# Kernel tuning notes

Measured on AMD Instinct MI355X. Metric: run time of the kernel, lower is better.

The kernel has to match this reference:

```python
import jax, jax.numpy as jnp
import numpy as np

V = 100000   # nodes (atoms)
E = 400000   # directed edges (bonds x2)
N = 74       # node_feat_size
NE = 12      # edge_feat_size
G = 200      # graph_feat_size
L = 2        # num_layers - 1 GNN layers
OUT = 1      # output_size
NG = 4000    # molecules in the batch


def _lin_init(k, fan_in, fan_out):
    s = 1.0 / np.sqrt(fan_in)
    return jax.random.uniform(k, (fan_in, fan_out), jnp.float32, -s, s)


def setup_inputs() -> dict:
    key = jax.random.key(0)
    ks = list(jax.random.split(key, 40))
    p = {}
    # node feats uniform in (0.05, 0.95) so mask = 1/(sum(h[:,-4:])*(1-h[:,0])) - 1 is finite
    p["node_feats"] = jax.random.uniform(ks[0], (V, N), jnp.float32, 0.05, 0.95)
    p["edge_feats"] = jax.random.normal(ks[1], (E, NE), jnp.float32)
    # GetContext params
    p["pn_W"] = _lin_init(ks[2], N, G);            p["pn_b"] = jnp.zeros((G,), jnp.float32)
    p["pe1_W"] = _lin_init(ks[3], N + NE, G);      p["pe1_b"] = jnp.zeros((G,), jnp.float32)
    p["pe2_W"] = _lin_init(ks[4], 2 * G, 1);       p["pe2_b"] = jnp.zeros((1,), jnp.float32)
    p["et_W"] = _lin_init(ks[5], G, G);            p["et_b"] = jnp.zeros((G,), jnp.float32)
    p["gru0_Wih"] = _lin_init(ks[6], G, 3 * G);    p["gru0_Whh"] = _lin_init(ks[7], G, 3 * G)
    p["gru0_bih"] = jnp.zeros((3 * G,), jnp.float32)
    p["gru0_bhh"] = jnp.zeros((3 * G,), jnp.float32)
    # stacked GNNLayer params
    p["gnn_pe_W"] = jnp.stack([_lin_init(ks[8 + l], 2 * G, 1) for l in range(L)])
    p["gnn_pe_b"] = jnp.zeros((L, 1), jnp.float32)
    p["gnn_pn_W"] = jnp.stack([_lin_init(ks[10 + l], G, G) for l in range(L)])
    p["gnn_pn_b"] = jnp.zeros((L, G), jnp.float32)
    p["gnn_gru_Wih"] = jnp.stack([_lin_init(ks[12 + l], G, 3 * G) for l in range(L)])
    p["gnn_gru_Whh"] = jnp.stack([_lin_init(ks[14 + l], G, 3 * G) for l in range(L)])
    p["gnn_gru_bih"] = jnp.zeros((L, 3 * G), jnp.float32)
    p["gnn_gru_bhh"] = jnp.zeros((L, 3 * G), jnp.float32)
    p["pred_W"] = _lin_init(ks[16], G, OUT);       p["pred_b"] = jnp.zeros((OUT,), jnp.float32)
    # graph structure
    p["src"] = jax.random.randint(ks[17], (E,), 0, V)
    p["dst"] = jax.random.randint(ks[18], (E,), 0, V)
    p["graph_ids"] = jnp.arange(V, dtype=jnp.int32) // (V // NG)  # sorted, balanced, non-empty
    p["n_graphs"] = NG
    return p


def _edge_softmax(logits, dst, num_nodes):
    # softmax over incoming edges of each destination node (DGL edge_softmax)
    m = jax.ops.segment_max(logits, dst, num_segments=num_nodes)
    e = jnp.exp(logits - m[dst])
    s = jax.ops.segment_sum(e, dst, num_segments=num_nodes)
    return e / s[dst]


def _gru_cell(x, h, Wih, Whh, bih, bhh):
    gi = x @ Wih + bih
    gh = h @ Whh + bhh
    ir, iz, inn = jnp.split(gi, 3, axis=-1)
    hr, hz, hn = jnp.split(gh, 3, axis=-1)
    r = jax.nn.sigmoid(ir + hr)
    z = jax.nn.sigmoid(iz + hz)
    n = jnp.tanh(inn + r * hn)
    return (1.0 - z) * n + z * h


def _forward(node_feats, edge_feats, pn_W, pn_b, pe1_W, pe1_b, pe2_W, pe2_b,
             et_W, et_b, gru0_Wih, gru0_Whh, gru0_bih, gru0_bhh,
             gnn_pe_W, gnn_pe_b, gnn_pn_W, gnn_pn_b,
             gnn_gru_Wih, gnn_gru_Whh, gnn_gru_bih, gnn_gru_bhh,
             pred_W, pred_b, src, dst, graph_ids, n_graphs):
    Vn = node_feats.shape[0]
    lrelu = jax.nn.leaky_relu  # slope 0.01, matches torch default
    # mask from original node features g.ndata['h']
    mask = jnp.sum(node_feats[:, -4:], axis=1) * (1.0 - node_feats[:, 0])
    mask = 1.0 / mask - 1.0
    # --- GetContext ---
    hv_new = lrelu(node_feats @ pn_W + pn_b)                               # (V, G)
    he1 = lrelu(jnp.concatenate([node_feats[src], edge_feats], 1) @ pe1_W + pe1_b)  # (E, G)
    he2 = jnp.concatenate([hv_new[dst], he1], 1)                           # (E, 2G)
    logits = lrelu(he2 @ pe2_W + pe2_b)                                    # (E, 1)
    a = _edge_softmax(logits, dst, Vn)
    e = a * (he1 @ et_W + et_b)                                            # (E, G)
    c = jax.ops.segment_sum(e, dst, num_segments=Vn)                       # (V, G)
    nf = jax.nn.relu(_gru_cell(jax.nn.elu(c), hv_new,
                               gru0_Wih, gru0_Whh, gru0_bih, gru0_bhh))
    # --- GNN layers ---
    for l in range(gnn_pe_W.shape[0]):
        he = jnp.concatenate([nf[dst], nf[src]], 1)                        # (E, 2G)
        lg = lrelu(he @ gnn_pe_W[l] + gnn_pe_b[l])                         # (E, 1)
        a = _edge_softmax(lg, dst, Vn)
        hvp = nf @ gnn_pn_W[l] + gnn_pn_b[l]                               # (V, G)
        c = jax.ops.segment_sum(hvp[src] * a, dst, num_segments=Vn)        # (V, G)
        nf = jax.nn.relu(_gru_cell(jax.nn.elu(c), nf,
                                   gnn_gru_Wih[l], gnn_gru_Whh[l],
                                   gnn_gru_bih[l], gnn_gru_bhh[l]))
    # --- readout ---
    atom_pka = nf @ pred_W + pred_b                                        # (V, 1)
    atom_pka = -(atom_pka + mask[:, None])
    h_pow = jnp.power(10.0, atom_pka)
    g_feats = -jnp.log10(jax.ops.segment_sum(h_pow, graph_ids, num_segments=n_graphs))
    atom_pka_out = -atom_pka
    return g_feats, atom_pka_out


def reference(node_feats, edge_feats, pn_W, pn_b, pe1_W, pe1_b, pe2_W, pe2_b,
              et_W, et_b, gru0_Wih, gru0_Whh, gru0_bih, gru0_bhh,
              gnn_pe_W, gnn_pe_b, gnn_pn_W, gnn_pn_b,
              gnn_gru_Wih, gnn_gru_Whh, gnn_gru_bih, gnn_gru_bhh,
              pred_W, pred_b, src, dst, graph_ids, n_graphs):
    return _forward(node_feats, edge_feats, pn_W, pn_b, pe1_W, pe1_b, pe2_W, pe2_b,
                    et_W, et_b, gru0_Wih, gru0_Whh, gru0_bih, gru0_bhh,
                    gnn_pe_W, gnn_pe_b, gnn_pn_W, gnn_pn_b,
                    gnn_gru_Wih, gnn_gru_Whh, gnn_gru_bih, gnn_gru_bhh,
                    pred_W, pred_b, src, dst, graph_ids, n_graphs)
```

## Files before the change

### kernel.cpp

```cpp
#include <hip/hip_runtime.h>
#include <hip/hip_bf16.h>
#include <math.h>

#define V_N    100000
#define E_N    400000
#define NFEAT  74
#define NEFEAT 12
#define G_DIM  200
#define LDA    224
#define L_N    2
#define NG_N   4000
#define NROWB  391
#define NROWP  392
#define NSWZ   (NROWP / 8 * 56)
#define NSWZG  (NROWP / 8 * 112)

static inline int cdiv(int a, int b) { return (a + b - 1) / b; }

__device__ __forceinline__ float lrelu_f(float x) { return x > 0.f ? x : 0.01f * x; }
__device__ __forceinline__ float sigmoid_f(float x)
{
    return __builtin_amdgcn_rcpf(1.f + __expf(-x));
}
__device__ __forceinline__ float tanh_f(float x)
{
    return 1.f - 2.f * __builtin_amdgcn_rcpf(__expf(2.f * x) + 1.f);
}
__device__ __forceinline__ float elu_f(float x) { return x > 0.f ? x : __expf(x) - 1.f; }
__device__ __forceinline__ float bf2f(__hip_bfloat16 x) { return __bfloat162float(x); }
__device__ __forceinline__ float bfbits2f(short s) {
    return __uint_as_float(((unsigned)(unsigned short)s) << 16);
}

__device__ __forceinline__ short f2bf(float f) {
    __hip_bfloat16 b = __float2bfloat16(f);
    short s;
    __builtin_memcpy(&s, &b, 2);
    return s;
}

typedef short short8 __attribute__((ext_vector_type(8)));
typedef short short4v __attribute__((ext_vector_type(4)));
typedef float f32x4 __attribute__((ext_vector_type(4)));

#define MFMA16(a, b, c) __builtin_amdgcn_mfma_f32_16x16x32_bf16((a), (b), (c), 0, 0, 0)

#define GLOAD_LDS16(gp, lp) \
    __builtin_amdgcn_global_load_lds((const __attribute__((address_space(1))) void*)(gp), \
                                     (__attribute__((address_space(3))) void*)(lp), 16, 0, 0)

#define WAITVM(n) do { \
    asm volatile("s_waitcnt vmcnt(" #n ")" ::: "memory"); \
    __builtin_amdgcn_sched_barrier(0); \
} while (0)

__device__ __forceinline__ void swz_decode7(int lin, int& rowBlk, int& cb)
{
    int grp = lin / 56;
    int rem = lin % 56;
    cb = rem >> 3;
    rowBlk = grp * 8 + (rem & 7);
}

__device__ __forceinline__ void swz_decode14(int lin, int& rowBlk, int& cb)
{
    int grp = lin / 112;
    int rem = lin % 112;
    cb = rem >> 3;
    rowBlk = grp * 8 + (rem & 7);
}

__device__ __forceinline__ f32x4 qcalc(const f32x4* wef, f32x4 ef0, f32x4 ef1, f32x4 ef2)
{
    f32x4 q = ef0[0] * wef[0];
    q += ef0[1] * wef[1];
    q += ef0[2] * wef[2];
    q += ef0[3] * wef[3];
    q += ef1[0] * wef[4];
    q += ef1[1] * wef[5];
    q += ef1[2] * wef[6];
    q += ef1[3] * wef[7];
    q += ef2[0] * wef[8];
    q += ef2[1] * wef[9];
    q += ef2[2] * wef[10];
    q += ef2[3] * wef[11];
    return q;
}

__global__ __launch_bounds__(256)
void fill_kernel(float* __restrict__ p, float v, int n)
{
    int i = blockIdx.x * blockDim.x + threadIdx.x;
    if (i < n) p[i] = v;
}

__global__ __launch_bounds__(256)
void fill_int_kernel(int* __restrict__ p, int v, int n)
{
    int i = blockIdx.x * blockDim.x + threadIdx.x;
    if (i < n) p[i] = v;
}

__global__ __launch_bounds__(256)
void pad_zero_kernel(short* __restrict__ base, size_t VP)
{
    int idx = blockIdx.x * blockDim.x + threadIdx.x;
    if (idx >= 4 * V_N) return;
    int mat = idx / V_N, row = idx % V_N;
    short* p = base + (size_t)mat * VP + (long)row * LDA + G_DIM;
    short8 z = {};
    *(short8*)(p) = z;
    *(short8*)(p + 8) = z;
    *(short8*)(p + 16) = z;
}

__global__ __launch_bounds__(256)
void wprep_kernel(const float* __restrict__ W, short* __restrict__ Wp, int K, int Kpad)
{
    int idx = blockIdx.x * 256 + threadIdx.x;
    if (idx >= 256 * Kpad) return;
    int j = idx / Kpad, k = idx % Kpad;
    float v = (j < G_DIM && k < K) ? W[(long)k * G_DIM + j] : 0.f;
    Wp[idx] = f2bf(v);
}

__global__ __launch_bounds__(256)
void wprep_tiled_kernel(const float* __restrict__ W, short* __restrict__ Wp)
{
    int idx = blockIdx.x * 256 + threadIdx.x;
    if (idx >= 7 * 7 * 1024) return;
    int cb = idx / (7 * 1024);
    int r = idx % (7 * 1024);
    int st = r / 1024;
    int r2 = r % 1024;
    int cc = r2 / 32, kk = r2 % 32;
    int col = cb * 32 + cc, k = st * 32 + kk;
    float v = (col < G_DIM && k < G_DIM) ? W[(long)k * G_DIM + col] : 0.f;
    Wp[idx] = f2bf(v);
}

__global__ __launch_bounds__(256)
void gru_wprep_kernel(const float* __restrict__ Wih, const float* __restrict__ Whh,
                      short* __restrict__ Wp)
{
    int idx = blockIdx.x * 256 + threadIdx.x;
    if (idx >= 14 * 14 * 1536) return;
    int cb = idx / (14 * 1536);
    int r = idx % (14 * 1536);
    int st = r / 1536;
    int r2 = r % 1536;
    int g = r2 / 512;
    int r3 = r2 % 512;
    int cc = r3 / 32, kk = r3 % 32;
    int col = cb * 16 + cc;
    float v = 0.f;
    if (col < G_DIM) {
        if (st < 7) {
            int k = st * 32 + kk;
            if (k < G_DIM) v = Wih[(long)k * (3 * G_DIM) + g * G_DIM + col];
        } else {
            int k = (st - 7) * 32 + kk;
            if (k < G_DIM) v = Whh[(long)k * (3 * G_DIM) + g * G_DIM + col];
        }
    }
    Wp[idx] = f2bf(v);
}

__global__ __launch_bounds__(256)
void hist_kernel(const int* __restrict__ dst, int* __restrict__ deg)
{
    int e = blockIdx.x * blockDim.x + threadIdx.x;
    if (e >= E_N) return;
    atomicAdd(&deg[dst[e]], 1);
}

__global__ __launch_bounds__(256)
void scan1_kernel(const int* __restrict__ deg, int* __restrict__ rp, int* __restrict__ bsum)
{
    __shared__ int s[256];
    int tid = threadIdx.x;
    int v = blockIdx.x * 256 + tid;
    int x = (v < V_N) ? deg[v] : 0;
    s[tid] = x;
    __syncthreads();
    for (int off = 1; off < 256; off <<= 1) {
        int t = (tid >= off) ? s[tid - off] : 0;
        __syncthreads();
        s[tid] += t;
        __syncthreads();
    }
    if (v < V_N) rp[v] = s[tid] - x;
    if (tid == 255) bsum[blockIdx.x] = s[255];
}

__global__ void scan2_kernel(int* __restrict__ bsum, int* __restrict__ rp, int nb)
{
    if (threadIdx.x != 0 || blockIdx.x != 0) return;
    int acc = 0;
    for (int b = 0; b < nb; b++) { int t = bsum[b]; bsum[b] = acc; acc += t; }
    rp[V_N] = acc;
}

__global__ __launch_bounds__(256)
void scan3_kernel(int* __restrict__ rp, const int* __restrict__ bsum)
{
    int v = blockIdx.x * 256 + threadIdx.x;
    if (v < V_N) rp[v] += bsum[v >> 8];
}

__global__ __launch_bounds__(256)
void csr_fill_kernel(const int* __restrict__ dst, const int* __restrict__ rp,
                     int* __restrict__ cnt, int* __restrict__ perm)
{
    int e = blockIdx.x * blockDim.x + threadIdx.x;
    if (e >= E_N) return;
    int d = dst[e];
    int pos = rp[d] + atomicAdd(&cnt[d], 1);
    perm[pos] = e;
}

__global__ __launch_bounds__(256)
void gemm_f32a_dual_kernel(const float* __restrict__ Af32,
                           const short* __restrict__ Wp1, const float* __restrict__ b1,
                           const short* __restrict__ Wp2, const float* __restrict__ b2,
                           __hip_bfloat16* __restrict__ C1,
                           __hip_bfloat16* __restrict__ C2)
{
    __shared__ short As[64 * 40];
    __shared__ short Bs1[64 * 40];
    __shared__ short Bs2[64 * 40];
    const int tid = threadIdx.x;
    const int lane = tid & 63;
    const int w = tid >> 6;
    const int quad = lane >> 4;
    const int lm = lane & 15;
    const int rowBase = blockIdx.y * 64;
    const int j0 = blockIdx.x * 64;
    const int arow = tid >> 2;
    const int akc = (tid & 3) * 8;
    const int agrow = rowBase + arow;

    f32x4 acc1[4] = {}, acc2[4] = {};

    for (int k0 = 0; k0 < 96; k0 += 32) {
        short8 av = {};
        if (agrow < V_N) {
            int gk = k0 + akc;
            #pragma unroll
            for (int i = 0; i < 8; i++) {
                int kg = gk + i;
                av[i] = (kg < NFEAT) ? f2bf(Af32[(long)agrow * NFEAT + kg]) : (short)0;
            }
        }
        *(short8*)&As[arow * 40 + akc] = av;
        {
            int col = tid >> 2;
            *(short8*)&Bs1[col * 40 + akc] =
                *(const short8*)(Wp1 + (long)(j0 + col) * 96 + k0 + akc);
            *(short8*)&Bs2[col * 40 + akc] =
                *(const short8*)(Wp2 + (long)(j0 + col) * 96 + k0 + akc);
        }
        __syncthreads();
        short8 a = *(short8*)&As[(w * 16 + lm) * 40 + quad * 8];
        #pragma unroll
        for (int nt = 0; nt < 4; nt++) {
            short8 bb1 = *(short8*)&Bs1[(nt * 16 + lm) * 40 + quad * 8];
            short8 bb2 = *(short8*)&Bs2[(nt * 16 + lm) * 40 + quad * 8];
            acc1[nt] = MFMA16(a, bb1, acc1[nt]);
            acc2[nt] = MFMA16(a, bb2, acc2[nt]);
        }
        __syncthreads();
    }

    #pragma unroll
    for (int nt = 0; nt < 4; nt++) {
        int col = j0 + nt * 16 + lm;
        if (col >= G_DIM) continue;
        float bv1 = b1[col], bv2 = b2[col];
        #pragma unroll
        for (int r = 0; r < 4; r++) {
            int grow = rowBase + w * 16 + quad * 4 + r;
            if (grow >= V_N) continue;
            C1[(long)grow * LDA + col] = __float2bfloat16(lrelu_f(acc1[nt][r] + bv1));
            C2[(long)grow * LDA + col] = __float2bfloat16(acc2[nt][r] + bv2);
        }
    }
}

template<int EPI>
__global__ __launch_bounds__(256)
void gemm_bf16a_kernel(const __hip_bfloat16* __restrict__ Abf,
                       const short* __restrict__ Wp,
                       const float* __restrict__ bias,
                       __hip_bfloat16* __restrict__ Cbf)
{
    __shared__ short As[2][256 * 32];
    int rowBlk, cb;
    swz_decode7(blockIdx.x, rowBlk, cb);
    if (rowBlk >= NROWB) return;
    const int tid = threadIdx.x;
    const int lane = tid & 63;
    const int w = tid >> 6;
    const int quad = lane >> 4;
    const int lm = lane & 15;
    const int j0 = cb * 32;
    const int rowBase = rowBlk * 256;

    const short* WpB = Wp + (long)cb * (7 * 1024);
    const short* As_g = (const short*)Abf;
    const long aoff = (long)(rowBase + w * 64 + (lane >> 2)) * LDA + (lane & 3) * 8;
    const int bfrag = lm * 32 + quad * 8;

    auto stageA = [&](int st, int buf) {
        const int kl = st * 32;
        #pragma unroll
        for (int c = 0; c < 4; c++)
            GLOAD_LDS16(As_g + aoff + (long)c * 16 * LDA + kl,
                        &As[buf][(w * 64 + c * 16) * 32]);
    };
    auto loadB = [&](int st, short8 bf[2]) {
        const short* bp = WpB + st * 1024 + bfrag;
        #pragma unroll
        for (int nt = 0; nt < 2; nt++)
            bf[nt] = *(const short8*)(bp + nt * 512);
    };
    auto mfmaStep = [&](int buf, short8 bf[2], f32x4 acc[4][2]) {
        #pragma unroll
        for (int rt = 0; rt < 4; rt++) {
            short8 a = *(short8*)&As[buf][(w * 64 + rt * 16 + lm) * 32 + quad * 8];
            acc[rt][0] = MFMA16(a, bf[0], acc[rt][0]);
            acc[rt][1] = MFMA16(a, bf[1], acc[rt][1]);
        }
    };

    f32x4 acc[4][2] = {};
    short8 bA[2], bB[2];

    stageA(0, 0);
    loadB(0, bA);
    WAITVM(0);

    #pragma unroll 1
    for (int st = 0; st < 7; st += 2) {
        if (st + 1 < 7) {
            stageA(st + 1, 1);
            loadB(st + 1, bB);
            WAITVM(6);
        } else {
            WAITVM(0);
        }
        mfmaStep(0, bA, acc);
        if (st + 1 < 7) {
            if (st + 2 < 7) {
                stageA(st + 2, 0);
                loadB(st + 2, bA);
                WAITVM(6);
            } else {
                WAITVM(0);
            }
            mfmaStep(1, bB, acc);
        }
    }

    #pragma unroll
    for (int nt = 0; nt < 2; nt++) {
        int col = j0 + nt * 16 + lm;
        if (col >= G_DIM) continue;
        float bv = bias[col];
        #pragma unroll
        for (int rt = 0; rt < 4; rt++) {
            #pragma unroll
            for (int r = 0; r < 4; r++) {
                int grow = rowBase + w * 64 + rt * 16 + quad * 4 + r;
                if (grow >= V_N) continue;
                float v = acc[rt][nt][r] + bv;
                if (EPI == 3) v = elu_f(v);
                Cbf[(long)grow * LDA + col] = __float2bfloat16(v);
            }
        }
    }
}

__global__ __launch_bounds__(256, 3)
void gru_mfma_kernel(const __hip_bfloat16* __restrict__ xc,
                     const __hip_bfloat16* __restrict__ h,
                     const short* __restrict__ Wp,
                     const float* __restrict__ bih, const float* __restrict__ bhh,
                     __hip_bfloat16* __restrict__ out)
{
    __shared__ short As[2][256 * 32];
    int rowBlk, cb;
    swz_decode14(blockIdx.x, rowBlk, cb);
    if (rowBlk >= NROWB) return;
    const int tid = threadIdx.x;
    const int lane = tid & 63;
    const int w = tid >> 6;
    const int quad = lane >> 4;
    const int lm = lane & 15;
    const int j0 = cb * 16;
    const int rowBase = rowBlk * 256;

    const short* WpB = Wp + (long)cb * (14 * 1536);
    const short* xc_s = (const short*)xc;
    const short* h_s = (const short*)h;
    const long aoff = (long)(rowBase + w * 64 + (lane >> 2)) * LDA + (lane & 3) * 8;
    const int bfrag = lm * 32 + quad * 8;

    auto stageA = [&](int st, int buf) {
        const short* Ap = (st < 7) ? xc_s : h_s;
        const int kl = (st < 7 ? st : st - 7) * 32;
        #pragma unroll
        for (int c = 0; c < 4; c++)
            GLOAD_LDS16(Ap + aoff + (long)c * 16 * LDA + kl,
                        &As[buf][(w * 64 + c * 16) * 32]);
    };
    auto loadB = [&](int st, short8 bf[3]) {
        const short* bp = WpB + st * 1536 + bfrag;
        #pragma unroll
        for (int g = 0; g < 3; g++)
            bf[g] = *(const short8*)(bp + g * 512);
    };

    f32x4 aR[4] = {}, aZ[4] = {}, aNl[4] = {}, aNh[4] = {};

    auto mfmaStep = [&](int buf, short8 bf[3], bool lowK) {
        #pragma unroll
        for (int rt = 0; rt < 4; rt++) {
            short8 a = *(short8*)&As[buf][(w * 64 + rt * 16 + lm) * 32 + quad * 8];
            aR[rt] = MFMA16(a, bf[0], aR[rt]);
            aZ[rt] = MFMA16(a, bf[1], aZ[rt]);
            if (lowK) aNl[rt] = MFMA16(a, bf[2], aNl[rt]);
            else      aNh[rt] = MFMA16(a, bf[2], aNh[rt]);
        }
    };

    short8 bA[3], bB[3];

    stageA(0, 0);
    loadB(0, bA);
    WAITVM(0);

    #pragma unroll 1
    for (int st = 0; st < 14; st += 2) {
        stageA(st + 1, 1);
        loadB(st + 1, bB);
        WAITVM(7);
        mfmaStep(0, bA, st < 7);
        if (st + 2 < 14) {
            stageA(st + 2, 0);
            loadB(st + 2, bA);
            WAITVM(7);
        } else {
            WAITVM(0);
        }
        mfmaStep(1, bB, st + 1 < 7);
    }

    int col = j0 + lm;
    if (col < G_DIM) {
        float b_r = bih[col] + bhh[col];
        float b_z = bih[G_DIM + col] + bhh[G_DIM + col];
        float b_in = bih[2 * G_DIM + col];
        float b_hn = bhh[2 * G_DIM + col];
        #pragma unroll
        for (int rt = 0; rt < 4; rt++) {
            #pragma unroll
            for (int r = 0; r < 4; r++) {
                int grow = rowBase + w * 64 + rt * 16 + quad * 4 + r;
                if (grow >= V_N) continue;
                float rr = sigmoid_f(aR[rt][r] + b_r);
                float zz = sigmoid_f(aZ[rt][r] + b_z);
                float nn = tanh_f(aNl[rt][r] + b_in + rr * (aNh[rt][r] + b_hn));
                float hval = bf2f(h[(long)grow * LDA + col]);
                float o = (1.f - zz) * nn + zz * hval;
                out[(long)grow * LDA + col] = __float2bfloat16(o > 0.f ? o : 0.f);
            }
        }
    }
}

__global__ __launch_bounds__(256)
void node_dot2_kernel(const __hip_bfloat16* __restrict__ X,
                      const float* __restrict__ wa, const float* __restrict__ wb,
                      float* __restrict__ s1, float* __restrict__ s2)
{
    int w = threadIdx.x >> 6, lane = threadIdx.x & 63;
    int v = blockIdx.x * 4 + w;
    if (v >= V_N) return;
    int vlane = (lane < 50) ? lane : 0;
    short4v pv = *(const short4v*)((const short*)X + (long)v * LDA + vlane * 4);
    f32x4 wav = *(const f32x4*)(wa + vlane * 4);
    float a = 0.f, b = 0.f;
    #pragma unroll
    for (int u = 0; u < 4; u++) a += bfbits2f(pv[u]) * wav[u];
    if (wb) {
        f32x4 wbv = *(const f32x4*)(wb + vlane * 4);
        #pragma unroll
        for (int u = 0; u < 4; u++) b += bfbits2f(pv[u]) * wbv[u];
    }
    if (lane >= 50) { a = 0.f; b = 0.f; }
    for (int off = 32; off > 0; off >>= 1) {
        a += __shfl_down(a, off, 64);
        if (wb) b += __shfl_down(b, off, 64);
    }
    if (lane == 0) {
        s1[v] = a;
        if (wb) s2[v] = b;
    }
}

__global__ __launch_bounds__(256)
void ctx_fused_kernel(const __hip_bfloat16* __restrict__ P,
                      const float* __restrict__ efeat,
                      const int* __restrict__ src,
                      const int* __restrict__ rp, const int* __restrict__ perm,
                      const float* __restrict__ s1,
                      const float* __restrict__ pe1W,
                      const float* __restrict__ pe2W, const float* __restrict__ pe2b,
                      __hip_bfloat16* __restrict__ hbar)
{
    const int tid = threadIdx.x;
    const int w = tid >> 6, lane = tid & 63;
    const int vlane = (lane < 50) ? lane : 0;
    const int v = __builtin_amdgcn_readfirstlane(blockIdx.x * 4 + w);
    if (v >= V_N) return;
    const int b = __builtin_amdgcn_readfirstlane(rp[v]);
    const int en = __builtin_amdgcn_readfirstlane(rp[v + 1]);
    if (en == b) {
        if (lane < 50) {
            short4v z = {};
            *(short4v*)((short*)hbar + (long)v * LDA + lane * 4) = z;
        }
        return;
    }
    f32x4 wef[12];
    #pragma unroll
    for (int j = 0; j < 12; j++)
        wef[j] = *(const f32x4*)(pe1W + (long)(NFEAT + j) * G_DIM + vlane * 4);
    const f32x4 w2 = *(const f32x4*)(pe2W + G_DIM + vlane * 4);
    const float s1b = s1[v] + pe2b[0];

    float m = -INFINITY, ssum = 0.f;
    f32x4 a = {};
    for (int i = b; i < en; i++) {
        const int e = __builtin_amdgcn_readfirstlane(perm[i]);
        const int sN = __builtin_amdgcn_readfirstlane(src[e]);
        const f32x4 ef0 = *(const f32x4*)(efeat + (long)e * NEFEAT);
        const f32x4 ef1 = *(const f32x4*)(efeat + (long)e * NEFEAT + 4);
        const f32x4 ef2 = *(const f32x4*)(efeat + (long)e * NEFEAT + 8);
        const short4v pv = *(const short4v*)((const short*)P + (long)sN * LDA + vlane * 4);
        const f32x4 q = qcalc(wef, ef0, ef1, ef2);
        f32x4 he;
        #pragma unroll
        for (int u = 0; u < 4; u++) he[u] = lrelu_f(bfbits2f(pv[u]) + q[u]);
        float dot = he[0] * w2[0] + he[1] * w2[1] + he[2] * w2[2] + he[3] * w2[3];
        if (lane >= 50) dot = 0.f;
        #pragma unroll
        for (int off = 32; off > 0; off >>= 1) dot += __shfl_xor(dot, off, 64);
        const float l = lrelu_f(dot + s1b);
        if (l <= m) {
            const float wgt = __expf(l - m);
            ssum += wgt;
            #pragma unroll
            for (int u = 0; u < 4; u++) a[u] += wgt * he[u];
        } else {
            const float scale = __expf(m - l);
            ssum = ssum * scale + 1.f;
            #pragma unroll
            for (int u = 0; u < 4; u++) a[u] = a[u] * scale + he[u];
            m = l;
        }
    }
    const float inv = __builtin_amdgcn_rcpf(ssum);
    if (lane < 50) {
        short4v o;
        #pragma unroll
        for (int u = 0; u < 4; u++) o[u] = f2bf(a[u] * inv);
        *(short4v*)((short*)hbar + (long)v * LDA + lane * 4) = o;
    }
}

__global__ __launch_bounds__(256)
void gnn_fused_agg_kernel(const __hip_bfloat16* __restrict__ X,
                          const int* __restrict__ src,
                          const int* __restrict__ rp, const int* __restrict__ perm,
                          const float* __restrict__ s1, const float* __restrict__ s2,
                          const float* __restrict__ bias,
                          __hip_bfloat16* __restrict__ out)
{
    const int tid = threadIdx.x;
    const int w = tid >> 6, lane = tid & 63;
    const int vlane = (lane < 50) ? lane : 0;
    const int v = __builtin_amdgcn_readfirstlane(blockIdx.x * 4 + w);
    if (v >= V_N) return;
    const int b = __builtin_amdgcn_readfirstlane(rp[v]);
    const int en = __builtin_amdgcn_readfirstlane(rp[v + 1]);
    if (en == b) {
        if (lane < 50) {
            short4v z = {};
            *(short4v*)((short*)out + (long)v * LDA + lane * 4) = z;
        }
        return;
    }
    const float s1v = s1[v] + bias[0];
    float m = -INFINITY;
    for (int i = b; i < en; i++) {
        const int e = __builtin_amdgcn_readfirstlane(perm[i]);
        const int sN = __builtin_amdgcn_readfirstlane(src[e]);
        m = fmaxf(m, lrelu_f(s1v + s2[sN]));
    }
    f32x4 a = {};
    float ssum = 0.f;
    for (int i = b; i < en; i++) {
        const int e = __builtin_amdgcn_readfirstlane(perm[i]);
        const int sN = __builtin_amdgcn_readfirstlane(src[e]);
        const float l = lrelu_f(s1v + s2[sN]);
        const float wgt = __expf(l - m);
        ssum += wgt;
        const short4v pv = *(const short4v*)((const short*)X + (long)sN * LDA + vlane * 4);
        #pragma unroll
        for (int u = 0; u < 4; u++)
            a[u] += wgt * bfbits2f(pv[u]);
    }
    const float inv = __builtin_amdgcn_rcpf(ssum);
    if (lane < 50) {
        short4v o;
        #pragma unroll
        for (int u = 0; u < 4; u++) o[u] = f2bf(elu_f(a[u] * inv));
        *(short4v*)((short*)out + (long)v * LDA + lane * 4) = o;
    }
}

__global__ __launch_bounds__(256)
void mask_kernel(const float* __restrict__ nfeat, float* __restrict__ mask)
{
    int v = blockIdx.x * blockDim.x + threadIdx.x;
    if (v >= V_N) return;
    const float* row = nfeat + (long)v * NFEAT;
    float s = row[NFEAT - 4] + row[NFEAT - 3] + row[NFEAT - 2] + row[NFEAT - 1];
    float m = s * (1.f - row[0]);
    mask[v] = 1.f / m - 1.f;
}

__global__ __launch_bounds__(256)
void readout_kernel(const __hip_bfloat16* __restrict__ nf, const float* __restrict__ predW,
                    const float* __restrict__ predb, const float* __restrict__ mask,
                    const int* __restrict__ gid, float* __restrict__ out_atom,
                    float* __restrict__ gsum)
{
    int gtid = blockIdx.x * blockDim.x + threadIdx.x;
    int v = gtid >> 6, lane = gtid & 63;
    if (v >= V_N) return;
    int vlane = (lane < 50) ? lane : 0;
    short4v pv = *(const short4v*)((const short*)nf + (long)v * LDA + vlane * 4);
    f32x4 wv = *(const f32x4*)(predW + vlane * 4);
    float acc = 0.f;
    #pragma unroll
    for (int u = 0; u < 4; u++) acc += bfbits2f(pv[u]) * wv[u];
    if (lane >= 50) acc = 0.f;
    for (int off = 32; off > 0; off >>= 1) acc += __shfl_down(acc, off, 64);
    if (lane == 0) {
        float p = acc + predb[0] + mask[v];
        out_atom[v] = p;
        atomicAdd(&gsum[gid[v]], exp10f(-p));
    }
}

__global__ __launch_bounds__(256)
void graph_out_kernel(const float* __restrict__ gsum, float* __restrict__ out_g)
{
    int g = blockIdx.x * blockDim.x + threadIdx.x;
    if (g >= NG_N) return;
    out_g[g] = -log10f(gsum[g]);
}

extern "C" void kernel_launch(void* const* d_in, const int* in_sizes, int n_in,
                              void* d_out, int out_size, void* d_ws, size_t ws_size,
                              hipStream_t stream)
{
    const float* node_feats = (const float*)d_in[0];
    const float* edge_feats = (const float*)d_in[1];
    const float* pn_W  = (const float*)d_in[2];
    const float* pn_b  = (const float*)d_in[3];
    const float* pe1_W = (const float*)d_in[4];
    const float* pe1_b = (const float*)d_in[5];
    const float* pe2_W = (const float*)d_in[6];
    const float* pe2_b = (const float*)d_in[7];
    const float* et_W  = (const float*)d_in[8];
    const float* et_b  = (const float*)d_in[9];
    const float* gru0_Wih = (const float*)d_in[10];
    const float* gru0_Whh = (const float*)d_in[11];
    const float* gru0_bih = (const float*)d_in[12];
    const float* gru0_bhh = (const float*)d_in[13];
    const float* gnn_pe_W = (const float*)d_in[14];
    const float* gnn_pe_b = (const float*)d_in[15];
    const float* gnn_pn_W = (const float*)d_in[16];
    const float* gnn_pn_b = (const float*)d_in[17];
    const float* gnn_gru_Wih = (const float*)d_in[18];
    const float* gnn_gru_Whh = (const float*)d_in[19];
    const float* gnn_gru_bih = (const float*)d_in[20];
    const float* gnn_gru_bhh = (const float*)d_in[21];
    const float* pred_W = (const float*)d_in[22];
    const float* pred_b = (const float*)d_in[23];
    const int* src = (const int*)d_in[24];
    const int* dst = (const int*)d_in[25];
    const int* gid = (const int*)d_in[26];

    float* out_g = (float*)d_out;
    float* out_atom = out_g + NG_N;

    char* base = (char*)d_ws;
    size_t off = 0;
    auto take = [&](size_t bytes) -> void* {
        void* p = base + off;
        off += (bytes + 255) & ~(size_t)255;
        return p;
    };
    const size_t VP = (size_t)V_N * LDA;
    const size_t WPL = (size_t)14 * 14 * 1536;
    float* mask   = (float*)take((size_t)V_N * 4);
    float* s1     = (float*)take((size_t)V_N * 4);
    float* s2     = (float*)take((size_t)V_N * 4);
    float* gsum   = (float*)take((size_t)NG_N * 4);
    __hip_bfloat16* c    = (__hip_bfloat16*)take(VP * 2);
    __hip_bfloat16* hv   = (__hip_bfloat16*)take(VP * 2);
    __hip_bfloat16* nf_a = (__hip_bfloat16*)take(VP * 2);
    __hip_bfloat16* nf_b = (__hip_bfloat16*)take(VP * 2);
    short* WpGru = (short*)take(3 * WPL * 2);
    short* Wp_pn0 = (short*)take((size_t)256 * 96 * 2);
    short* Wp_pe1 = (short*)take((size_t)256 * 96 * 2);
    short* Wp_et  = (short*)take((size_t)7 * 7 * 1024 * 2);
    short* Wp_pn1 = (short*)take((size_t)7 * 7 * 1024 * 2);
    short* Wp_pn2 = (short*)take((size_t)7 * 7 * 1024 * 2);
    int* deg  = (int*)take((size_t)V_N * 4);
    int* cnt  = (int*)take((size_t)V_N * 4);
    int* rp   = (int*)take((size_t)(V_N + 1) * 4);
    int* perm = (int*)take((size_t)E_N * 4);
    int* bsum = (int*)take((size_t)512 * 4);
    __hip_bfloat16* P    = nf_a;
    __hip_bfloat16* hbar = nf_b;
    __hip_bfloat16* hvp  = hv;

    if (off > ws_size) {
        fill_kernel<<<cdiv(out_size, 256), 256, 0, stream>>>((float*)d_out, -12345.f, out_size);
        return;
    }

    const int BLK = 256;
    const int nScanBlocks = cdiv(V_N, 256);
    const dim3 gOld(4, cdiv(V_N, 64));
    const int gAgg = cdiv(V_N, 4);

    pad_zero_kernel<<<cdiv(4 * V_N, BLK), BLK, 0, stream>>>((short*)c, VP);

    gru_wprep_kernel<<<cdiv(14 * 14 * 1536, 256), BLK, 0, stream>>>(gru0_Wih, gru0_Whh, WpGru);
    for (int l = 0; l < L_N; l++)
        gru_wprep_kernel<<<cdiv(14 * 14 * 1536, 256), BLK, 0, stream>>>(
            gnn_gru_Wih + (size_t)l * G_DIM * 3 * G_DIM,
            gnn_gru_Whh + (size_t)l * G_DIM * 3 * G_DIM,
            WpGru + (size_t)(l + 1) * WPL);
    wprep_kernel<<<cdiv(256 * 96, 256), BLK, 0, stream>>>(pn_W, Wp_pn0, NFEAT, 96);
    wprep_kernel<<<cdiv(256 * 96, 256), BLK, 0, stream>>>(pe1_W, Wp_pe1, NFEAT, 96);
    wprep_tiled_kernel<<<cdiv(7 * 7 * 1024, 256), BLK, 0, stream>>>(et_W, Wp_et);
    wprep_tiled_kernel<<<cdiv(7 * 7 * 1024, 256), BLK, 0, stream>>>(gnn_pn_W, Wp_pn1);
    wprep_tiled_kernel<<<cdiv(7 * 7 * 1024, 256), BLK, 0, stream>>>(
        gnn_pn_W + (size_t)G_DIM * G_DIM, Wp_pn2);

    mask_kernel<<<cdiv(V_N, BLK), BLK, 0, stream>>>(node_feats, mask);

    fill_int_kernel<<<cdiv(V_N, BLK), BLK, 0, stream>>>(deg, 0, V_N);
    hist_kernel<<<cdiv(E_N, BLK), BLK, 0, stream>>>(dst, deg);
    scan1_kernel<<<nScanBlocks, BLK, 0, stream>>>(deg, rp, bsum);
    scan2_kernel<<<1, 1, 0, stream>>>(bsum, rp, nScanBlocks);
    scan3_kernel<<<nScanBlocks, BLK, 0, stream>>>(rp, bsum);
    fill_int_kernel<<<cdiv(V_N, BLK), BLK, 0, stream>>>(cnt, 0, V_N);
    csr_fill_kernel<<<cdiv(E_N, BLK), BLK, 0, stream>>>(dst, rp, cnt, perm);

    gemm_f32a_dual_kernel<<<gOld, BLK, 0, stream>>>(
        node_feats, Wp_pn0, pn_b, Wp_pe1, pe1_b, hv, P);
    node_dot2_kernel<<<gAgg, BLK, 0, stream>>>(hv, pe2_W, nullptr, s1, nullptr);
    ctx_fused_kernel<<<gAgg, BLK, 0, stream>>>(
        P, edge_feats, src, rp, perm, s1, pe1_W, pe2_W, pe2_b, hbar);
    gemm_bf16a_kernel<3><<<NSWZ, BLK, 0, stream>>>(hbar, Wp_et, et_b, c);
    gru_mfma_kernel<<<NSWZG, BLK, 0, stream>>>(c, hv, WpGru, gru0_bih, gru0_bhh, nf_a);

    __hip_bfloat16* cur = nf_a;
    __hip_bfloat16* nxt = nf_b;
    for (int l = 0; l < L_N; l++) {
        const float* pe_W = gnn_pe_W + (size_t)l * 2 * G_DIM;
        const float* pe_b = gnn_pe_b + l;
        const float* pnB  = gnn_pn_b + (size_t)l * G_DIM;
        const float* bih  = gnn_gru_bih + (size_t)l * 3 * G_DIM;
        const float* bhh  = gnn_gru_bhh + (size_t)l * 3 * G_DIM;
        const short* WpPn = (l == 0) ? Wp_pn1 : Wp_pn2;

        node_dot2_kernel<<<gAgg, BLK, 0, stream>>>(cur, pe_W, pe_W + G_DIM, s1, s2);
        gemm_bf16a_kernel<1><<<NSWZ, BLK, 0, stream>>>(cur, WpPn, pnB, hvp);
        gnn_fused_agg_kernel<<<gAgg, BLK, 0, stream>>>(
            hvp, src, rp, perm, s1, s2, pe_b, c);
        gru_mfma_kernel<<<NSWZG, BLK, 0, stream>>>(
            c, cur, WpGru + (size_t)(l + 1) * WPL, bih, bhh, nxt);

        __hip_bfloat16* tmp = cur; cur = nxt; nxt = tmp;
    }

    fill_kernel<<<cdiv(NG_N, BLK), BLK, 0, stream>>>(gsum, 0.f, NG_N);
    readout_kernel<<<cdiv(V_N * 64, BLK), BLK, 0, stream>>>(
        cur, pred_W, pred_b, mask, gid, out_atom, gsum);
    graph_out_kernel<<<cdiv(NG_N, BLK), BLK, 0, stream>>>(gsum, out_g);
}
```

Before: 1.197 ms.

## Batch edge index loads per wavefront and prefetch next neighbor row in aggregation

In both attention aggregation kernels, each lane now loads one edge's perm/src index for a chunk of up to 64 edges, and the indices are broadcast with shuffles. This replaces the serial dependent scalar loads done per edge. The next edge's features and source-node row are software-prefetched while the current edge is processed. The GNN kernel also computes its attention logits in parallel across lanes and uses a chunked online softmax with wave reductions, which removes the separate max pass over edges. This adds shuffle and register cost and slightly changes the floating-point summation order.

```diff
diff --git a/kernel.cpp b/kernel.cpp
--- a/kernel.cpp
+++ b/kernel.cpp
@@ -542,33 +542,52 @@
 
     float m = -INFINITY, ssum = 0.f;
     f32x4 a = {};
-    for (int i = b; i < en; i++) {
-        const int e = __builtin_amdgcn_readfirstlane(perm[i]);
-        const int sN = __builtin_amdgcn_readfirstlane(src[e]);
-        const f32x4 ef0 = *(const f32x4*)(efeat + (long)e * NEFEAT);
-        const f32x4 ef1 = *(const f32x4*)(efeat + (long)e * NEFEAT + 4);
-        const f32x4 ef2 = *(const f32x4*)(efeat + (long)e * NEFEAT + 8);
-        const short4v pv = *(const short4v*)((const short*)P + (long)sN * LDA + vlane * 4);
-        const f32x4 q = qcalc(wef, ef0, ef1, ef2);
-        f32x4 he;
-        #pragma unroll
-        for (int u = 0; u < 4; u++) he[u] = lrelu_f(bfbits2f(pv[u]) + q[u]);
-        float dot = he[0] * w2[0] + he[1] * w2[1] + he[2] * w2[2] + he[3] * w2[3];
-        if (lane >= 50) dot = 0.f;
-        #pragma unroll
-        for (int off = 32; off > 0; off >>= 1) dot += __shfl_xor(dot, off, 64);
-        const float l = lrelu_f(dot + s1b);
-        if (l <= m) {
-            const float wgt = __expf(l - m);
-            ssum += wgt;
+    for (int cb0 = b; cb0 < en; cb0 += 64) {
+        int i = cb0 + lane;
+        int eL = 0, sL = 0;
+        if (i < en) { eL = perm[i]; sL = src[eL]; }
+        const int cnt = min(64, en - cb0);
+        int sT = __shfl(sL, 0, 64);
+        int eT = __shfl(eL, 0, 64);
+        f32x4 ef0 = *(const f32x4*)(efeat + (long)eT * NEFEAT);
+        f32x4 ef1 = *(const f32x4*)(efeat + (long)eT * NEFEAT + 4);
+        f32x4 ef2 = *(const f32x4*)(efeat + (long)eT * NEFEAT + 8);
+        short4v pv = *(const short4v*)((const short*)P + (long)sT * LDA + vlane * 4);
+        for (int t = 0; t < cnt; t++) {
+            f32x4 nef0, nef1, nef2;
+            short4v npv;
+            if (t + 1 < cnt) {
+                int sN = __shfl(sL, t + 1, 64);
+                int eN = __shfl(eL, t + 1, 64);
+                nef0 = *(const f32x4*)(efeat + (long)eN * NEFEAT);
+                nef1 = *(const f32x4*)(efeat + (long)eN * NEFEAT + 4);
+                nef2 = *(const f32x4*)(efeat + (long)eN * NEFEAT + 8);
+                npv = *(const short4v*)((const short*)P + (long)sN * LDA + vlane * 4);
+            }
+            const f32x4 q = qcalc(wef, ef0, ef1, ef2);
+            f32x4 he;
             #pragma unroll
-            for (int u = 0; u < 4; u++) a[u] += wgt * he[u];
-        } else {
-            const float scale = __expf(m - l);
-            ssum = ssum * scale + 1.f;
+            for (int u = 0; u < 4; u++) he[u] = lrelu_f(bfbits2f(pv[u]) + q[u]);
+            float dot = he[0] * w2[0] + he[1] * w2[1] + he[2] * w2[2] + he[3] * w2[3];
+            if (lane >= 50) dot = 0.f;
             #pragma unroll
-            for (int u = 0; u < 4; u++) a[u] = a[u] * scale + he[u];
-            m = l;
+            for (int off = 32; off > 0; off >>= 1) dot += __shfl_xor(dot, off, 64);
+            const float l = lrelu_f(dot + s1b);
+            if (l <= m) {
+                const float wgt = __expf(l - m);
+                ssum += wgt;
+                #pragma unroll
+                for (int u = 0; u < 4; u++) a[u] += wgt * he[u];
+            } else {
+                const float scale = __expf(m - l);
+                ssum = ssum * scale + 1.f;
+                #pragma unroll
+                for (int u = 0; u < 4; u++) a[u] = a[u] * scale + he[u];
+                m = l;
+            }
+            if (t + 1 < cnt) {
+                ef0 = nef0; ef1 = nef1; ef2 = nef2; pv = npv;
+            }
         }
     }
     const float inv = __builtin_amdgcn_rcpf(ssum);
@@ -603,24 +622,48 @@
         return;
     }
     const float s1v = s1[v] + bias[0];
-    float m = -INFINITY;
-    for (int i = b; i < en; i++) {
-        const int e = __builtin_amdgcn_readfirstlane(perm[i]);
-        const int sN = __builtin_amdgcn_readfirstlane(src[e]);
-        m = fmaxf(m, lrelu_f(s1v + s2[sN]));
-    }
+    float m = -INFINITY, ssum = 0.f;
     f32x4 a = {};
-    float ssum = 0.f;
-    for (int i = b; i < en; i++) {
-        const int e = __builtin_amdgcn_readfirstlane(perm[i]);
-        const int sN = __builtin_amdgcn_readfirstlane(src[e]);
-        const float l = lrelu_f(s1v + s2[sN]);
-        const float wgt = __expf(l - m);
-        ssum += wgt;
-        const short4v pv = *(const short4v*)((const short*)X + (long)sN * LDA + vlane * 4);
-        #pragma unroll
-        for (int u = 0; u < 4; u++)
-            a[u] += wgt * bfbits2f(pv[u]);
+    for (int cb0 = b; cb0 < en; cb0 += 64) {
+        int i = cb0 + lane;
+        int sL = 0;
+        float lv = -INFINITY;
+        if (i < en) {
+            int e = perm[i];
+            sL = src[e];
+            lv = lrelu_f(s1v + s2[sL]);
+        }
+        float cm = lv;
+        #pragma unroll
+        for (int off = 32; off > 0; off >>= 1) cm = fmaxf(cm, __shfl_xor(cm, off, 64));
+        const float m_new = fmaxf(m, cm);
+        const float scale = __expf(m - m_new);
+        ssum *= scale;
+        #pragma unroll
+        for (int u = 0; u < 4; u++) a[u] *= scale;
+        float wgt = (i < en) ? __expf(lv - m_new) : 0.f;
+        float ws = wgt;
+        #pragma unroll
+        for (int off = 32; off > 0; off >>= 1) ws += __shfl_xor(ws, off, 64);
+        ssum += ws;
+        const int cnt = min(64, en - cb0);
+        int sT = __shfl(sL, 0, 64);
+        float wT = __shfl(wgt, 0, 64);
+        short4v pv = *(const short4v*)((const short*)X + (long)sT * LDA + vlane * 4);
+        for (int t = 0; t < cnt; t++) {
+            short4v npv;
+            float wN;
+            if (t + 1 < cnt) {
+                int sN = __shfl(sL, t + 1, 64);
+                wN = __shfl(wgt, t + 1, 64);
+                npv = *(const short4v*)((const short*)X + (long)sN * LDA + vlane * 4);
+            }
+            #pragma unroll
+            for (int u = 0; u < 4; u++)
+                a[u] += wT * bfbits2f(pv[u]);
+            if (t + 1 < cnt) { pv = npv; wT = wN; }
+        }
+        m = m_new;
     }
     const float inv = __builtin_amdgcn_rcpf(ssum);
     if (lane < 50) {
```

New measurement: 1.176 ms. About the same (-1.8%).
